# Optimization experiments

Measured on AMD Instinct MI355X. Metric: run time of the kernel, lower is better.

The kernel has to match this reference:

```python
import jax, jax.numpy as jnp
import numpy as np

EPS_SINKHORN = 0.01   # entropic regularization (cost / eps)
EPS_LOG = 1e-8        # numerical epsilon inside logs
NUM_ITERS = 50


def setup_inputs() -> dict:
    key = jax.random.key(0)
    k1, k2 = jax.random.split(key)
    B, N = 8, 2048
    x1 = jax.random.normal(k1, (B, N, 3), dtype=jnp.float32)
    x2 = jax.random.normal(k2, (B, N, 3), dtype=jnp.float32)
    return {"x1": x1, "x2": x2}


def reference(x1, x2):
    # x1, x2: [B, N, 3] point clouds
    B, N, _ = x1.shape
    # pairwise squared-distance cost matrix: [B, N, N]
    cost = jnp.sum((x1[:, :, None, :] - x2[:, None, :, :]) ** 2, axis=-1)
    K = jnp.exp(-cost / EPS_SINKHORN)  # constant across iterations

    inv_n = jnp.float32(1.0 / N)
    mu = jnp.full((B, N), inv_n, dtype=cost.dtype)
    nu = jnp.full((B, N), inv_n, dtype=cost.dtype)
    log_mu = jnp.log(mu + EPS_LOG)
    log_nu = jnp.log(nu + EPS_LOG)

    def step(carry, _):
        u, v = carry
        # row update: sum_j K_ij * exp(v_j)
        u = log_mu - jnp.log(jnp.einsum('bij,bj->bi', K, jnp.exp(v)) + EPS_LOG)
        # col update: sum_i K_ij * exp(u_i)
        v = log_nu - jnp.log(jnp.einsum('bij,bi->bj', K, jnp.exp(u)) + EPS_LOG)
        return (u, v), None

    u0 = jnp.zeros((B, N), dtype=cost.dtype)
    v0 = jnp.zeros((B, N), dtype=cost.dtype)
    (u, v), _ = jax.lax.scan(step, (u0, v0), None, length=NUM_ITERS)

    transport = K * jnp.exp(u[:, :, None] + v[:, None, :])  # [B, N, N]
    emd = jnp.sum(transport * cost, axis=(1, 2))            # [B]
    return emd
```

## Files before the change

kernel.cpp:

```cpp
#include <hip/hip_runtime.h>
#include <cmath>

#define BATCH 8
#define NPT   2048
#define NPAIR (NPT / 2)
#define NPTS  (BATCH * NPT)
#define TILES 64
#define GRID_MAIN 256
#define THREADS 1024
#define ITERS 50

#define C_LOG2E 1.4426950408889634f
#define NEG100C (-144.26950408889634f)
#define S200C   288.53900817779268f
#define EPS_LOG 1e-8f
#define LN2_01  0.006931471805599453f

typedef float v2f __attribute__((ext_vector_type(2)));
typedef float v4f __attribute__((ext_vector_type(4)));
typedef unsigned long long u64t;

static __device__ __forceinline__ float fast_exp2(float x) {
#if __has_builtin(__builtin_amdgcn_exp2f)
    return __builtin_amdgcn_exp2f(x);
#else
    return exp2f(x);
#endif
}

static __device__ __forceinline__ v2f pk_fma(v2f a, v2f b, v2f c) {
    v2f d;
    asm("v_pk_fma_f32 %0, %1, %2, %3" : "=v"(d) : "v"(a), "v"(b), "v"(c));
    return d;
}
static __device__ __forceinline__ v2f pk_add(v2f a, v2f b) {
    v2f d;
    asm("v_pk_add_f32 %0, %1, %2" : "=v"(d) : "v"(a), "v"(b));
    return d;
}

static __device__ __forceinline__ float gload(const float* p) {
    return __hip_atomic_load(p, __ATOMIC_RELAXED, __HIP_MEMORY_SCOPE_AGENT);
}
static __device__ __forceinline__ void gstore(float* p, float val) {
    __hip_atomic_store(p, val, __ATOMIC_RELAXED, __HIP_MEMORY_SCOPE_AGENT);
}
static __device__ __forceinline__ u64t gload2(const float* p) {
    return __hip_atomic_load((const u64t*)p, __ATOMIC_RELAXED,
                             __HIP_MEMORY_SCOPE_AGENT);
}

__global__ void init_kernel(float* __restrict__ out,
                            unsigned int* __restrict__ flags) {
    int t = threadIdx.x;
    if (t < BATCH) out[t] = 0.0f;
    flags[t] = 0u;
}

static __device__ __forceinline__ void bar_arrive(unsigned int* flags,
                                                  int slot, unsigned int ph) {
    __syncthreads();
    if (threadIdx.x == 0)
        __hip_atomic_store(&flags[slot], ph, __ATOMIC_RELAXED,
                           __HIP_MEMORY_SCOPE_AGENT);
}
static __device__ __forceinline__ void bar_wait(const unsigned int* bflags,
                                                int wave, int lane,
                                                unsigned int ph) {
    if (wave == 0) {
        while (__hip_atomic_load(&bflags[lane], __ATOMIC_RELAXED,
                                 __HIP_MEMORY_SCOPE_AGENT) < ph) {
            __builtin_amdgcn_s_sleep(1);
        }
    }
    __syncthreads();
    __builtin_amdgcn_sched_barrier(0);
}

static __device__ __forceinline__ float half_core(
        const v4f* cdXY, const v4f* cdZW, int p0,
        v2f RX, v2f RY, v2f RZ, v2f RC)
{
    float accx = 0.0f, accy = 0.0f;
#pragma unroll 4
    for (int s = 0; s < 32; s++) {
        v4f a  = cdXY[p0 + s];
        v4f bz = cdZW[p0 + s];
        v2f xx = __builtin_shufflevector(a,  a,  0, 1);
        v2f yy = __builtin_shufflevector(a,  a,  2, 3);
        v2f zz = __builtin_shufflevector(bz, bz, 0, 1);
        v2f ww = __builtin_shufflevector(bz, bz, 2, 3);
        v2f t = pk_fma(xx, RX, ww);
        t = pk_fma(yy, RY, t);
        t = pk_fma(zz, RZ, t);
        t = pk_add(t, RC);
        accx += fast_exp2(t.x);
        accy += fast_exp2(t.y);
    }
    return accx + accy;
}

__global__ __launch_bounds__(THREADS, 4) void sinkhorn_kernel(
        const float* __restrict__ x1, const float* __restrict__ x2,
        float* __restrict__ u, float* __restrict__ v,
        unsigned int* __restrict__ flags, float* __restrict__ out)
{
    __shared__ v4f c1XY[2][NPAIR], c1ZW[2][NPAIR];
    __shared__ v4f c2XY[2][NPAIR], c2ZW[2][NPAIR];
    __shared__ float part[32][17];

    const int b0   = blockIdx.x / TILES;
    const int tile = blockIdx.x % TILES;
    const int bA = b0, bB = b0 + 4;
    const int baseA = bA * NPT, baseB = bB * NPT;
    const int slotA = bA * TILES + tile, slotB = bB * TILES + tile;
    const unsigned int* flA = flags + bA * TILES;
    const unsigned int* flB = flags + bB * TILES;

    const int tid  = threadIdx.x;
    const int wave = tid >> 6;
    const int lane = tid & 63;
    const int rloc = lane & 31;
    const int ch   = lane >> 5;
    const int row  = tile * 32 + rloc;
    const int p0   = wave * 64 + ch * 32;

    const float log_mu = logf(1.0f / (float)NPT + EPS_LOG);

    float P1a[2], P1b[2], P2a[2], P2b[2];
#pragma unroll
    for (int g = 0; g < 2; g++) {
        int base = g ? baseB : baseA;
        const float* p = x1 + 3 * (base + 2 * tid);
        float ax = p[0], ay = p[1], az = p[2];
        float bx = p[3], by = p[4], bz = p[5];
        float na = fmaf(ax, ax, fmaf(ay, ay, az * az));
        float nb = fmaf(bx, bx, fmaf(by, by, bz * bz));
        P1a[g] = na * NEG100C;  P1b[g] = nb * NEG100C;
        c1XY[g][tid] = (v4f){ax * S200C, bx * S200C, ay * S200C, by * S200C};
        c1ZW[g][tid] = (v4f){az * S200C, bz * S200C, P1a[g], P1b[g]};

        p = x2 + 3 * (base + 2 * tid);
        ax = p[0]; ay = p[1]; az = p[2];
        bx = p[3]; by = p[4]; bz = p[5];
        na = fmaf(ax, ax, fmaf(ay, ay, az * az));
        nb = fmaf(bx, bx, fmaf(by, by, bz * bz));
        P2a[g] = na * NEG100C;  P2b[g] = nb * NEG100C;
        c2XY[g][tid] = (v4f){ax * S200C, bx * S200C, ay * S200C, by * S200C};
        c2ZW[g][tid] = (v4f){az * S200C, bz * S200C, P2a[g], P2b[g]};
    }

    v2f RX1[2], RY1[2], RZ1[2], RC1[2], RX2[2], RY2[2], RZ2[2], RC2[2];
    float rc1s[2];
#pragma unroll
    for (int g = 0; g < 2; g++) {
        int base = g ? baseB : baseA;
        const float* p = x1 + 3 * (base + row);
        float a = p[0], bb = p[1], c = p[2];
        float nn = NEG100C * fmaf(a, a, fmaf(bb, bb, c * c));
        RX1[g] = (v2f){a, a};  RY1[g] = (v2f){bb, bb};
        RZ1[g] = (v2f){c, c};  RC1[g] = (v2f){nn, nn};
        rc1s[g] = nn;
        p = x2 + 3 * (base + row);
        a = p[0]; bb = p[1]; c = p[2];
        nn = NEG100C * fmaf(a, a, fmaf(bb, bb, c * c));
        RX2[g] = (v2f){a, a};  RY2[g] = (v2f){bb, bb};
        RZ2[g] = (v2f){c, c};  RC2[g] = (v2f){nn, nn};
    }
    __syncthreads();

    unsigned int ph = 0;
    for (int it = 0; it < ITERS; it++) {
        if (it > 0) {
            u64t dA = gload2(v + baseA + 2 * tid);
            u64t dB = gload2(v + baseB + 2 * tid);
            reinterpret_cast<v2f*>(&c2ZW[0][tid])[1] = (v2f){
                fmaf(C_LOG2E, __uint_as_float((unsigned)dA), P2a[0]),
                fmaf(C_LOG2E, __uint_as_float((unsigned)(dA >> 32)), P2b[0])};
            reinterpret_cast<v2f*>(&c2ZW[1][tid])[1] = (v2f){
                fmaf(C_LOG2E, __uint_as_float((unsigned)dB), P2a[1]),
                fmaf(C_LOG2E, __uint_as_float((unsigned)(dB >> 32)), P2b[1])};
            __syncthreads();
        }
        {
            float s = half_core(c2XY[0], c2ZW[0], p0,
                                RX1[0], RY1[0], RZ1[0], RC1[0]);
            s += __shfl_xor(s, 32, 64);
            if (lane < 32) part[rloc][wave] = s;
            __syncthreads();
            if (wave == 0) {
                float t = 0.0f;
#pragma unroll
                for (int w = 0; w < 16; w++) t += part[rloc][w];
                float res = log_mu - __logf(t + EPS_LOG);
                if (lane < 32) gstore(&u[baseA + row], res);
            }
        }
        bar_arrive(flags, slotA, ph + 1);
        {
            float s = half_core(c2XY[1], c2ZW[1], p0,
                                RX1[1], RY1[1], RZ1[1], RC1[1]);
            s += __shfl_xor(s, 32, 64);
            if (lane < 32) part[rloc][wave] = s;
            __syncthreads();
            if (wave == 0) {
                float t = 0.0f;
#pragma unroll
                for (int w = 0; w < 16; w++) t += part[rloc][w];
                float res = log_mu - __logf(t + EPS_LOG);
                if (lane < 32) gstore(&u[baseB + row], res);
            }
        }
        bar_arrive(flags, slotB, ph + 1);
        bar_wait(flA, wave, lane, ph + 1);
        bar_wait(flB, wave, lane, ph + 1);
        {
            u64t dA = gload2(u + baseA + 2 * tid);
            u64t dB = gload2(u + baseB + 2 * tid);
            reinterpret_cast<v2f*>(&c1ZW[0][tid])[1] = (v2f){
                fmaf(C_LOG2E, __uint_as_float((unsigned)dA), P1a[0]),
                fmaf(C_LOG2E, __uint_as_float((unsigned)(dA >> 32)), P1b[0])};
            reinterpret_cast<v2f*>(&c1ZW[1][tid])[1] = (v2f){
                fmaf(C_LOG2E, __uint_as_float((unsigned)dB), P1a[1]),
                fmaf(C_LOG2E, __uint_as_float((unsigned)(dB >> 32)), P1b[1])};
            __syncthreads();
        }
        {
            float s = half_core(c1XY[0], c1ZW[0], p0,
                                RX2[0], RY2[0], RZ2[0], RC2[0]);
            s += __shfl_xor(s, 32, 64);
            if (lane < 32) part[rloc][wave] = s;
            __syncthreads();
            if (wave == 0) {
                float t = 0.0f;
#pragma unroll
                for (int w = 0; w < 16; w++) t += part[rloc][w];
                float res = log_mu - __logf(t + EPS_LOG);
                if (lane < 32) gstore(&v[baseA + row], res);
            }
        }
        bar_arrive(flags, slotA, ph + 2);
        {
            float s = half_core(c1XY[1], c1ZW[1], p0,
                                RX2[1], RY2[1], RZ2[1], RC2[1]);
            s += __shfl_xor(s, 32, 64);
            if (lane < 32) part[rloc][wave] = s;
            __syncthreads();
            if (wave == 0) {
                float t = 0.0f;
#pragma unroll
                for (int w = 0; w < 16; w++) t += part[rloc][w];
                float res = log_mu - __logf(t + EPS_LOG);
                if (lane < 32) gstore(&v[baseB + row], res);
            }
        }
        bar_arrive(flags, slotB, ph + 2);
        bar_wait(flA, wave, lane, ph + 2);
        bar_wait(flB, wave, lane, ph + 2);
        ph += 2;
    }

    v2f* cvp0 = reinterpret_cast<v2f*>(c1XY[0]);
    v2f* cvp1 = reinterpret_cast<v2f*>(c1XY[1]);
    {
        u64t dA = gload2(v + baseA + 2 * tid);
        u64t dB = gload2(v + baseB + 2 * tid);
        float aA = __uint_as_float((unsigned)dA);
        float bA2 = __uint_as_float((unsigned)(dA >> 32));
        float aB = __uint_as_float((unsigned)dB);
        float bB2 = __uint_as_float((unsigned)(dB >> 32));
        reinterpret_cast<v2f*>(&c2ZW[0][tid])[1] =
            (v2f){fmaf(C_LOG2E, aA, P2a[0]), fmaf(C_LOG2E, bA2, P2b[0])};
        reinterpret_cast<v2f*>(&c2ZW[1][tid])[1] =
            (v2f){fmaf(C_LOG2E, aB, P2a[1]), fmaf(C_LOG2E, bB2, P2b[1])};
        cvp0[tid] = (v2f){0.01f * aA, 0.01f * bA2};
        cvp1[tid] = (v2f){0.01f * aB, 0.01f * bB2};
    }
    __syncthreads();

    const v2f NL2 = {-LN2_01, -LN2_01};
    float es[2];
#pragma unroll
    for (int g = 0; g < 2; g++) {
        int base = g ? baseB : baseA;
        v2f* cvp = g ? cvp1 : cvp0;
        float ur = gload(&u[base + row]);
        float rcs = fmaf(C_LOG2E, ur, rc1s[g]);
        v2f RCC = (v2f){rcs, rcs};
        float sus = 0.01f * ur;
        v2f SU = (v2f){sus, sus};
        v2f eacc = {0.0f, 0.0f};
#pragma unroll 4
        for (int s = 0; s < 32; s++) {
            v4f a   = c2XY[g][p0 + s];
            v4f bz  = c2ZW[g][p0 + s];
            v2f cv2 = cvp[p0 + s];
            v2f xx = __builtin_shufflevector(a,  a,  0, 1);
            v2f yy = __builtin_shufflevector(a,  a,  2, 3);
            v2f zz = __builtin_shufflevector(bz, bz, 0, 1);
            v2f ww = __builtin_shufflevector(bz, bz, 2, 3);
            v2f t = pk_fma(xx, RX1[g], ww);
            t = pk_fma(yy, RY1[g], t);
            t = pk_fma(zz, RZ1[g], t);
            t = pk_add(t, RCC);
            v2f c2 = pk_fma(t, NL2, pk_add(SU, cv2));
            eacc.x = fmaf(fast_exp2(t.x), c2.x, eacc.x);
            eacc.y = fmaf(fast_exp2(t.y), c2.y, eacc.y);
        }
        float e = eacc.x + eacc.y;
#pragma unroll
        for (int m = 32; m >= 1; m >>= 1) e += __shfl_xor(e, m, 64);
        es[g] = e;
    }

    if (lane == 0) { part[0][wave] = es[0]; part[1][wave] = es[1]; }
    __syncthreads();
    if (tid == 0) {
        float sA = 0.0f, sB = 0.0f;
#pragma unroll
        for (int w = 0; w < 16; w++) { sA += part[0][w]; sB += part[1][w]; }
        atomicAdd(&out[bA], sA);
        atomicAdd(&out[bB], sB);
    }
}

extern "C" void kernel_launch(void* const* d_in, const int* in_sizes, int n_in,
                              void* d_out, int out_size, void* d_ws, size_t ws_size,
                              hipStream_t stream) {
    (void)in_sizes; (void)n_in; (void)out_size; (void)ws_size;
    const float* x1 = (const float*)d_in[0];
    const float* x2 = (const float*)d_in[1];
    float* out = (float*)d_out;

    char* ws = (char*)d_ws;
    float* u = (float*)ws;
    float* v = u + NPTS;
    unsigned int* flags = (unsigned int*)(v + NPTS);

    init_kernel<<<1, 512, 0, stream>>>(out, flags);
    sinkhorn_kernel<<<GRID_MAIN, THREADS, 0, stream>>>(x1, x2, u, v, flags, out);
}
```

Baseline: 829.8 us.

## Split grid barrier per batch half to overlap half A compute with half B wait

Restructures the Sinkhorn iteration loop so each half of the batch (slotA / slotB) waits only on its own barrier flag before folding u or v and computing the next update. Work on half A can start as soon as its group has arrived, while half B is still in flight, instead of waiting on both halves at once. The first u update is moved out of the loop and the last is skipped inside it, and the final v fold is no longer repeated in the epilogue. Correctness now depends on the per-half dependency ordering staying valid.

```diff
diff --git a/kernel.cpp b/kernel.cpp
--- a/kernel.cpp
+++ b/kernel.cpp
@@ -169,95 +169,60 @@
     }
     __syncthreads();
 
-    unsigned int ph = 0;
+    auto reduce_store = [&](float s, float* dst) {
+        s += __shfl_xor(s, 32, 64);
+        if (lane < 32) part[rloc][wave] = s;
+        __syncthreads();
+        if (wave == 0) {
+            float t = 0.0f;
+#pragma unroll
+            for (int w = 0; w < 16; w++) t += part[rloc][w];
+            float res = log_mu - __logf(t + EPS_LOG);
+            if (lane < 32) gstore(dst, res);
+        }
+    };
+    auto fold_u = [&](int g) {
+        u64t d = gload2(u + (g ? baseB : baseA) + 2 * tid);
+        reinterpret_cast<v2f*>(&c1ZW[g][tid])[1] = (v2f){
+            fmaf(C_LOG2E, __uint_as_float((unsigned)d), P1a[g]),
+            fmaf(C_LOG2E, __uint_as_float((unsigned)(d >> 32)), P1b[g])};
+        __syncthreads();
+    };
+    auto fold_v = [&](int g) {
+        u64t d = gload2(v + (g ? baseB : baseA) + 2 * tid);
+        reinterpret_cast<v2f*>(&c2ZW[g][tid])[1] = (v2f){
+            fmaf(C_LOG2E, __uint_as_float((unsigned)d), P2a[g]),
+            fmaf(C_LOG2E, __uint_as_float((unsigned)(d >> 32)), P2b[g])};
+        __syncthreads();
+    };
+    auto comp_u = [&](int g) {
+        float s = half_core(c2XY[g], c2ZW[g], p0,
+                            RX1[g], RY1[g], RZ1[g], RC1[g]);
+        reduce_store(s, u + (g ? baseB : baseA) + row);
+    };
+    auto comp_v = [&](int g) {
+        float s = half_core(c1XY[g], c1ZW[g], p0,
+                            RX2[g], RY2[g], RZ2[g], RC2[g]);
+        reduce_store(s, v + (g ? baseB : baseA) + row);
+    };
+
+    comp_u(0); bar_arrive(flags, slotA, 1);
+    comp_u(1); bar_arrive(flags, slotB, 1);
+
     for (int it = 0; it < ITERS; it++) {
-        if (it > 0) {
-            u64t dA = gload2(v + baseA + 2 * tid);
-            u64t dB = gload2(v + baseB + 2 * tid);
-            reinterpret_cast<v2f*>(&c2ZW[0][tid])[1] = (v2f){
-                fmaf(C_LOG2E, __uint_as_float((unsigned)dA), P2a[0]),
-                fmaf(C_LOG2E, __uint_as_float((unsigned)(dA >> 32)), P2b[0])};
-            reinterpret_cast<v2f*>(&c2ZW[1][tid])[1] = (v2f){
-                fmaf(C_LOG2E, __uint_as_float((unsigned)dB), P2a[1]),
-                fmaf(C_LOG2E, __uint_as_float((unsigned)(dB >> 32)), P2b[1])};
-            __syncthreads();
-        }
-        {
-            float s = half_core(c2XY[0], c2ZW[0], p0,
-                                RX1[0], RY1[0], RZ1[0], RC1[0]);
-            s += __shfl_xor(s, 32, 64);
-            if (lane < 32) part[rloc][wave] = s;
-            __syncthreads();
-            if (wave == 0) {
-                float t = 0.0f;
-#pragma unroll
-                for (int w = 0; w < 16; w++) t += part[rloc][w];
-                float res = log_mu - __logf(t + EPS_LOG);
-                if (lane < 32) gstore(&u[baseA + row], res);
-            }
-        }
-        bar_arrive(flags, slotA, ph + 1);
-        {
-            float s = half_core(c2XY[1], c2ZW[1], p0,
-                                RX1[1], RY1[1], RZ1[1], RC1[1]);
-            s += __shfl_xor(s, 32, 64);
-            if (lane < 32) part[rloc][wave] = s;
-            __syncthreads();
-            if (wave == 0) {
-                float t = 0.0f;
-#pragma unroll
-                for (int w = 0; w < 16; w++) t += part[rloc][w];
-                float res = log_mu - __logf(t + EPS_LOG);
-                if (lane < 32) gstore(&u[baseB + row], res);
-            }
-        }
-        bar_arrive(flags, slotB, ph + 1);
-        bar_wait(flA, wave, lane, ph + 1);
-        bar_wait(flB, wave, lane, ph + 1);
-        {
-            u64t dA = gload2(u + baseA + 2 * tid);
-            u64t dB = gload2(u + baseB + 2 * tid);
-            reinterpret_cast<v2f*>(&c1ZW[0][tid])[1] = (v2f){
-                fmaf(C_LOG2E, __uint_as_float((unsigned)dA), P1a[0]),
-                fmaf(C_LOG2E, __uint_as_float((unsigned)(dA >> 32)), P1b[0])};
-            reinterpret_cast<v2f*>(&c1ZW[1][tid])[1] = (v2f){
-                fmaf(C_LOG2E, __uint_as_float((unsigned)dB), P1a[1]),
-                fmaf(C_LOG2E, __uint_as_float((unsigned)(dB >> 32)), P1b[1])};
-            __syncthreads();
-        }
-        {
-            float s = half_core(c1XY[0], c1ZW[0], p0,
-                                RX2[0], RY2[0], RZ2[0], RC2[0]);
-            s += __shfl_xor(s, 32, 64);
-            if (lane < 32) part[rloc][wave] = s;
-            __syncthreads();
-            if (wave == 0) {
-                float t = 0.0f;
-#pragma unroll
-                for (int w = 0; w < 16; w++) t += part[rloc][w];
-                float res = log_mu - __logf(t + EPS_LOG);
-                if (lane < 32) gstore(&v[baseA + row], res);
-            }
-        }
-        bar_arrive(flags, slotA, ph + 2);
-        {
-            float s = half_core(c1XY[1], c1ZW[1], p0,
-                                RX2[1], RY2[1], RZ2[1], RC2[1]);
-            s += __shfl_xor(s, 32, 64);
-            if (lane < 32) part[rloc][wave] = s;
-            __syncthreads();
-            if (wave == 0) {
-                float t = 0.0f;
-#pragma unroll
-                for (int w = 0; w < 16; w++) t += part[rloc][w];
-                float res = log_mu - __logf(t + EPS_LOG);
-                if (lane < 32) gstore(&v[baseB + row], res);
-            }
-        }
-        bar_arrive(flags, slotB, ph + 2);
-        bar_wait(flA, wave, lane, ph + 2);
-        bar_wait(flB, wave, lane, ph + 2);
-        ph += 2;
+        const unsigned pu = 2 * it + 1, pv = 2 * it + 2;
+        bar_wait(flA, wave, lane, pu);
+        fold_u(0);
+        comp_v(0); bar_arrive(flags, slotA, pv);
+        bar_wait(flB, wave, lane, pu);
+        fold_u(1);
+        comp_v(1); bar_arrive(flags, slotB, pv);
+        bar_wait(flA, wave, lane, pv);
+        fold_v(0);
+        if (it < ITERS - 1) { comp_u(0); bar_arrive(flags, slotA, pu + 2); }
+        bar_wait(flB, wave, lane, pv);
+        fold_v(1);
+        if (it < ITERS - 1) { comp_u(1); bar_arrive(flags, slotB, pu + 2); }
     }
 
     v2f* cvp0 = reinterpret_cast<v2f*>(c1XY[0]);
@@ -265,16 +230,10 @@
     {
         u64t dA = gload2(v + baseA + 2 * tid);
         u64t dB = gload2(v + baseB + 2 * tid);
-        float aA = __uint_as_float((unsigned)dA);
-        float bA2 = __uint_as_float((unsigned)(dA >> 32));
-        float aB = __uint_as_float((unsigned)dB);
-        float bB2 = __uint_as_float((unsigned)(dB >> 32));
-        reinterpret_cast<v2f*>(&c2ZW[0][tid])[1] =
-            (v2f){fmaf(C_LOG2E, aA, P2a[0]), fmaf(C_LOG2E, bA2, P2b[0])};
-        reinterpret_cast<v2f*>(&c2ZW[1][tid])[1] =
-            (v2f){fmaf(C_LOG2E, aB, P2a[1]), fmaf(C_LOG2E, bB2, P2b[1])};
-        cvp0[tid] = (v2f){0.01f * aA, 0.01f * bA2};
-        cvp1[tid] = (v2f){0.01f * aB, 0.01f * bB2};
+        cvp0[tid] = (v2f){0.01f * __uint_as_float((unsigned)dA),
+                          0.01f * __uint_as_float((unsigned)(dA >> 32))};
+        cvp1[tid] = (v2f){0.01f * __uint_as_float((unsigned)dB),
+                          0.01f * __uint_as_float((unsigned)(dB >> 32))};
     }
     __syncthreads();
 
```

Result: no change. 825.3 us (-0.5%).
